# Optimization experiments

Hardware: AMD Instinct MI355X
Metric: run time of the kernel (lower is better)

The kernel has to match this reference:

```python
import jax, jax.numpy as jnp
import numpy as np

B, T, D, H, O = 8, 16, 113344, 512, 6


def setup_inputs() -> dict:
    key = jax.random.key(0)
    ks = jax.random.split(key, 11)
    k = 1.0 / np.sqrt(H)  # PyTorch nn.LSTM / nn.Linear default init scale
    u = lambda kk, shape: jax.random.uniform(kk, shape, jnp.float32, -k, k)
    x = jax.random.normal(ks[0], (B, T, D), jnp.float32)
    return dict(
        x=x,
        W_ih0=u(ks[1], (4 * H, D)), W_hh0=u(ks[2], (4 * H, H)),
        b_ih0=u(ks[3], (4 * H,)), b_hh0=u(ks[4], (4 * H,)),
        W_ih1=u(ks[5], (4 * H, H)), W_hh1=u(ks[6], (4 * H, H)),
        b_ih1=u(ks[7], (4 * H,)), b_hh1=u(ks[8], (4 * H,)),
        fc_w=u(ks[9], (O, H)), fc_b=u(ks[10], (O,)),
    )


def _lstm_layer(x, Wih, Whh, bih, bhh):
    # x: [B, T, D_in]; PyTorch gate order: i, f, g, o
    Bq = x.shape[0]
    Hq = Whh.shape[1]
    # Batch the input-to-hidden GEMM over all timesteps at once.
    xg = jnp.einsum('btd,gd->btg', x, Wih) + bih + bhh  # [B, T, 4H]

    def step(carry, xg_t):
        h, c = carry
        gates = xg_t + h @ Whh.T  # [B, 4H]
        i, f, g, o = jnp.split(gates, 4, axis=-1)
        i = jax.nn.sigmoid(i)
        f = jax.nn.sigmoid(f)
        g = jnp.tanh(g)
        o = jax.nn.sigmoid(o)
        c = f * c + i * g
        h = o * jnp.tanh(c)
        return (h, c), h

    h0 = jnp.zeros((Bq, Hq), x.dtype)
    c0 = jnp.zeros((Bq, Hq), x.dtype)
    (_, _), hs = jax.lax.scan(step, (h0, c0), jnp.swapaxes(xg, 0, 1))
    return jnp.swapaxes(hs, 0, 1)  # [B, T, H]


def reference(x, W_ih0, W_hh0, b_ih0, b_hh0, W_ih1, W_hh1, b_ih1, b_hh1, fc_w, fc_b):
    h = _lstm_layer(x, W_ih0, W_hh0, b_ih0, b_hh0)
    h = _lstm_layer(h, W_ih1, W_hh1, b_ih1, b_hh1)
    # fc on last timestep only
    return h[:, -1, :] @ fc_w.T + fc_b  # [B, O]
```

## Files before the change

kernel.cpp:

```cpp
#include <hip/hip_runtime.h>
#include <cstdint>
#include <cstddef>

typedef __attribute__((ext_vector_type(4))) float f32x4;
typedef __attribute__((ext_vector_type(8))) short s16x8;

#define MFMA16(a, b, c) __builtin_amdgcn_mfma_f32_16x16x32_bf16(a, b, c, 0, 0, 0)

__device__ __forceinline__ void bsplit(float f, unsigned short& h, unsigned short& l) {
  unsigned u = __float_as_uint(f);
  h = (unsigned short)(u >> 16);
  float hf = __uint_as_float(u & 0xffff0000u);
  l = (unsigned short)(__float_as_uint(f - hf) >> 16);
}

__device__ __forceinline__ void stage_tile(const float* __restrict__ base, int D, int k,
                                           unsigned short* ldsH, unsigned short* ldsL,
                                           int tid) {
#pragma unroll
  for (int v = 0; v < 4; ++v) {
    int flat = v * 256 + tid;
    int row = flat >> 3, kq = flat & 7;
    const float4 f = *(const float4*)(base + (size_t)row * D + k + kq * 4);
    ushort4 hh, ll;
    bsplit(f.x, hh.x, ll.x);
    bsplit(f.y, hh.y, ll.y);
    bsplit(f.z, hh.z, ll.z);
    bsplit(f.w, hh.w, ll.w);
    *(ushort4*)&ldsH[row * 40 + kq * 4] = hh;
    *(ushort4*)&ldsL[row * 40 + kq * 4] = ll;
  }
}

__global__ __launch_bounds__(256) void k_gemm(const float* __restrict__ A,
                                              const float* __restrict__ W,
                                              float* __restrict__ out,
                                              int D, int stepsPerChunk) {
  __shared__ __align__(16) unsigned short Ah[128 * 40], Al[128 * 40];
  __shared__ __align__(16) unsigned short Bh[128 * 40], Bl[128 * 40];
  const int tid = threadIdx.x;
  const int n0 = blockIdx.x * 128;
  const int totalSteps = D >> 5;
  const int s0 = blockIdx.y * stepsPerChunk;
  const int s1 = (s0 + stepsPerChunk < totalSteps) ? s0 + stepsPerChunk : totalSteps;
  const int wave = tid >> 6, lane = tid & 63;
  const int q = lane >> 4, li = lane & 15;
  const int wm = (wave >> 1) * 64, wn = (wave & 1) * 64;
  const float* bbase = W + (size_t)n0 * D;

  f32x4 acc[4][4] = {};

  for (int s = s0; s < s1; ++s) {
    const int k = s << 5;
    stage_tile(A, D, k, Ah, Al, tid);
    stage_tile(bbase, D, k, Bh, Bl, tid);
    __syncthreads();

    s16x8 a_h[4], a_l[4], b_h[4], b_l[4];
#pragma unroll
    for (int mt = 0; mt < 4; ++mt) {
      int m = wm + mt * 16 + li;
      a_h[mt] = *(const s16x8*)&Ah[m * 40 + q * 8];
      a_l[mt] = *(const s16x8*)&Al[m * 40 + q * 8];
    }
#pragma unroll
    for (int nt = 0; nt < 4; ++nt) {
      int n = wn + nt * 16 + li;
      b_h[nt] = *(const s16x8*)&Bh[n * 40 + q * 8];
      b_l[nt] = *(const s16x8*)&Bl[n * 40 + q * 8];
    }
#pragma unroll
    for (int mt = 0; mt < 4; ++mt)
#pragma unroll
      for (int nt = 0; nt < 4; ++nt) {
        acc[mt][nt] = MFMA16(a_h[mt], b_h[nt], acc[mt][nt]);
        acc[mt][nt] = MFMA16(a_h[mt], b_l[nt], acc[mt][nt]);
        acc[mt][nt] = MFMA16(a_l[mt], b_h[nt], acc[mt][nt]);
      }
    __syncthreads();
  }

#pragma unroll
  for (int mt = 0; mt < 4; ++mt)
#pragma unroll
    for (int nt = 0; nt < 4; ++nt)
#pragma unroll
      for (int r = 0; r < 4; ++r) {
        int m = wm + mt * 16 + q * 4 + r;
        int n = n0 + wn + nt * 16 + li;
        atomicAdd(&out[m * 2048 + n], acc[mt][nt][r]);
      }
}

__global__ __launch_bounds__(256) void k_rec(const float* __restrict__ xg,
                                             const float* __restrict__ Whh,
                                             const float* __restrict__ bih,
                                             const float* __restrict__ bhh,
                                             float* __restrict__ h_all,
                                             int* __restrict__ cnt) {
  __shared__ __align__(16) unsigned short Ah[16 * 520], Al[16 * 520];
  const int tid = threadIdx.x;
  const int lane = tid & 63, wave = tid >> 6;
  const int q = lane >> 4, li = lane & 15;
  const int g = li >> 2, jj = li & 3;
  const int wgl = blockIdx.x * 4 + wave;
  const int j0 = wgl * 4;
  const int row = g * 512 + j0 + jj;

  for (int i = tid; i < 16 * 520; i += 256) { Ah[i] = 0; Al[i] = 0; }

  s16x8 wh[16], wl[16];
#pragma unroll
  for (int ks = 0; ks < 16; ++ks) {
    float fv[8];
    *(float4*)&fv[0] = *(const float4*)(Whh + row * 512 + ks * 32 + q * 8);
    *(float4*)&fv[4] = *(const float4*)(Whh + row * 512 + ks * 32 + q * 8 + 4);
    s16x8 h8, l8;
#pragma unroll
    for (int j = 0; j < 8; ++j) {
      unsigned short h, l;
      bsplit(fv[j], h, l);
      h8[j] = (short)h;
      l8[j] = (short)l;
    }
    wh[ks] = h8;
    wl[ks] = l8;
  }
  const float bias = bih[row] + bhh[row];
  float c[4] = {0.f, 0.f, 0.f, 0.f};
  __syncthreads();

  for (int t = 0; t < 16; ++t) {
    if (t > 0) {
      if (tid == 0) {
        while (__hip_atomic_load(cnt + (t - 1), __ATOMIC_ACQUIRE,
                                 __HIP_MEMORY_SCOPE_AGENT) < (int)gridDim.x) {}
      }
      __syncthreads();
#pragma unroll
      for (int v = 0; v < 4; ++v) {
        int flat = v * 256 + tid;
        int b = flat >> 7, kq = flat & 127;
        float4 f = *(const float4*)(h_all + (b * 16 + (t - 1)) * 512 + kq * 4);
        ushort4 hh, ll;
        bsplit(f.x, hh.x, ll.x);
        bsplit(f.y, hh.y, ll.y);
        bsplit(f.z, hh.z, ll.z);
        bsplit(f.w, hh.w, ll.w);
        *(ushort4*)&Ah[b * 520 + kq * 4] = hh;
        *(ushort4*)&Al[b * 520 + kq * 4] = ll;
      }
      __syncthreads();
    }

    f32x4 acc = {0.f, 0.f, 0.f, 0.f};
    if (t > 0) {
#pragma unroll
      for (int ks = 0; ks < 16; ++ks) {
        s16x8 ah = *(const s16x8*)&Ah[li * 520 + ks * 32 + q * 8];
        s16x8 al = *(const s16x8*)&Al[li * 520 + ks * 32 + q * 8];
        acc = MFMA16(ah, wh[ks], acc);
        acc = MFMA16(ah, wl[ks], acc);
        acc = MFMA16(al, wh[ks], acc);
      }
    }

    float val[4];
#pragma unroll
    for (int r = 0; r < 4; ++r) {
      int mrow = q * 4 + r;
      float pre = acc[r] + bias;
      if (mrow < 8) pre += xg[(mrow * 16 + t) * 2048 + row];
      val[r] = (g == 2) ? tanhf(pre) : 1.f / (1.f + __expf(-pre));
    }
    const int base = lane & 48;
#pragma unroll
    for (int r = 0; r < 4; ++r) {
      float iv = __shfl(val[r], base + 0 + jj);
      float fv = __shfl(val[r], base + 4 + jj);
      float gv = __shfl(val[r], base + 8 + jj);
      float ov = __shfl(val[r], base + 12 + jj);
      int mrow = q * 4 + r;
      if (g == 0 && mrow < 8) {
        c[r] = fv * c[r] + iv * gv;
        float hv = ov * tanhf(c[r]);
        h_all[(mrow * 16 + t) * 512 + j0 + jj] = hv;
      }
    }

    if (t < 15) {
      __threadfence();
      __syncthreads();
      if (tid == 0)
        __hip_atomic_fetch_add(cnt + t, 1, __ATOMIC_RELEASE, __HIP_MEMORY_SCOPE_AGENT);
    }
  }
}

__global__ void k_fc(const float* __restrict__ h_all, const float* __restrict__ fw,
                     const float* __restrict__ fb, float* __restrict__ out) {
  int b = blockIdx.x / 6, o = blockIdx.x % 6;
  int lane = threadIdx.x;
  const float* h = h_all + (b * 16 + 15) * 512;
  float s = 0.f;
  for (int j = lane; j < 512; j += 64) s += h[j] * fw[o * 512 + j];
#pragma unroll
  for (int off = 32; off; off >>= 1) s += __shfl_down(s, off);
  if (lane == 0) out[b * 6 + o] = s + fb[o];
}

extern "C" void kernel_launch(void* const* d_in, const int* in_sizes, int n_in,
                              void* d_out, int out_size, void* d_ws, size_t ws_size,
                              hipStream_t stream) {
  const float* x    = (const float*)d_in[0];
  const float* Wih0 = (const float*)d_in[1];
  const float* Whh0 = (const float*)d_in[2];
  const float* bih0 = (const float*)d_in[3];
  const float* bhh0 = (const float*)d_in[4];
  const float* Wih1 = (const float*)d_in[5];
  const float* Whh1 = (const float*)d_in[6];
  const float* bih1 = (const float*)d_in[7];
  const float* bhh1 = (const float*)d_in[8];
  const float* fcw  = (const float*)d_in[9];
  const float* fcb  = (const float*)d_in[10];
  float* out = (float*)d_out;

  char* ws = (char*)d_ws;
  size_t off = 0;
  auto alloc = [&](size_t bytes) -> void* {
    void* p = ws + off;
    off += (bytes + 255) & ~(size_t)255;
    return p;
  };
  float* xg0 = (float*)alloc(128 * 2048 * sizeof(float));
  float* xg1 = (float*)alloc(128 * 2048 * sizeof(float));
  int* cnt   = (int*)alloc(4096);
  const size_t zeroBytes = off;
  float* h0 = (float*)alloc(128 * 512 * sizeof(float));
  float* h1 = (float*)alloc(128 * 512 * sizeof(float));
  (void)ws_size; (void)in_sizes; (void)n_in; (void)out_size;

  hipMemsetAsync(d_ws, 0, zeroBytes, stream);

  k_gemm<<<dim3(16, 77), 256, 0, stream>>>(x, Wih0, xg0, 113344, 46);
  k_rec<<<32, 256, 0, stream>>>(xg0, Whh0, bih0, bhh0, h0, cnt);

  k_gemm<<<dim3(16, 4), 256, 0, stream>>>(h0, Wih1, xg1, 512, 4);
  k_rec<<<32, 256, 0, stream>>>(xg1, Whh1, bih1, bhh1, h1, cnt + 16);

  k_fc<<<48, 64, 0, stream>>>(h1, fcw, fcb, out);
}
```

Baseline: 1.612 ms.

## Fuse both LSTM layers into one wavefront-pipelined kernel and prefetch GEMM tiles

```diff
diff --git a/kernel.cpp b/kernel.cpp
--- a/kernel.cpp
+++ b/kernel.cpp
@@ -14,14 +14,24 @@
   l = (unsigned short)(__float_as_uint(f - hf) >> 16);
 }
 
-__device__ __forceinline__ void stage_tile(const float* __restrict__ base, int D, int k,
-                                           unsigned short* ldsH, unsigned short* ldsL,
-                                           int tid) {
+
+__device__ __forceinline__ void load_tile(const float* __restrict__ base, int D, int k,
+                                          int tid, float4* r) {
 #pragma unroll
   for (int v = 0; v < 4; ++v) {
     int flat = v * 256 + tid;
     int row = flat >> 3, kq = flat & 7;
-    const float4 f = *(const float4*)(base + (size_t)row * D + k + kq * 4);
+    r[v] = *(const float4*)(base + (size_t)row * D + k + kq * 4);
+  }
+}
+
+__device__ __forceinline__ void write_tile(const float4* r, unsigned short* ldsH,
+                                           unsigned short* ldsL, int tid) {
+#pragma unroll
+  for (int v = 0; v < 4; ++v) {
+    int flat = v * 256 + tid;
+    int row = flat >> 3, kq = flat & 7;
+    float4 f = r[v];
     ushort4 hh, ll;
     bsplit(f.x, hh.x, ll.x);
     bsplit(f.y, hh.y, ll.y);
@@ -32,10 +42,10 @@
   }
 }
 
-__global__ __launch_bounds__(256) void k_gemm(const float* __restrict__ A,
-                                              const float* __restrict__ W,
-                                              float* __restrict__ out,
-                                              int D, int stepsPerChunk) {
+__global__ __launch_bounds__(256, 2) void k_gemm(const float* __restrict__ A,
+                                                 const float* __restrict__ W,
+                                                 float* __restrict__ out,
+                                                 int D, int stepsPerChunk) {
   __shared__ __align__(16) unsigned short Ah[128 * 40], Al[128 * 40];
   __shared__ __align__(16) unsigned short Bh[128 * 40], Bl[128 * 40];
   const int tid = threadIdx.x;
@@ -49,12 +59,18 @@
   const float* bbase = W + (size_t)n0 * D;
 
   f32x4 acc[4][4] = {};
+  float4 pa[4], pb[4];
+  load_tile(A, D, s0 << 5, tid, pa);
+  load_tile(bbase, D, s0 << 5, tid, pb);
 
   for (int s = s0; s < s1; ++s) {
-    const int k = s << 5;
-    stage_tile(A, D, k, Ah, Al, tid);
-    stage_tile(bbase, D, k, Bh, Bl, tid);
+    write_tile(pa, Ah, Al, tid);
+    write_tile(pb, Bh, Bl, tid);
     __syncthreads();
+    if (s + 1 < s1) {
+      load_tile(A, D, (s + 1) << 5, tid, pa);
+      load_tile(bbase, D, (s + 1) << 5, tid, pb);
+    }
 
     s16x8 a_h[4], a_l[4], b_h[4], b_l[4];
 #pragma unroll
@@ -92,29 +108,14 @@
       }
 }
 
-__global__ __launch_bounds__(256) void k_rec(const float* __restrict__ xg,
-                                             const float* __restrict__ Whh,
-                                             const float* __restrict__ bih,
-                                             const float* __restrict__ bhh,
-                                             float* __restrict__ h_all,
-                                             int* __restrict__ cnt) {
-  __shared__ __align__(16) unsigned short Ah[16 * 520], Al[16 * 520];
-  const int tid = threadIdx.x;
-  const int lane = tid & 63, wave = tid >> 6;
-  const int q = lane >> 4, li = lane & 15;
-  const int g = li >> 2, jj = li & 3;
-  const int wgl = blockIdx.x * 4 + wave;
-  const int j0 = wgl * 4;
-  const int row = g * 512 + j0 + jj;
-
-  for (int i = tid; i < 16 * 520; i += 256) { Ah[i] = 0; Al[i] = 0; }
-
-  s16x8 wh[16], wl[16];
+
+__device__ __forceinline__ void load_wfrags(const float* __restrict__ W, int row, int q,
+                                            s16x8* wh, s16x8* wl) {
 #pragma unroll
   for (int ks = 0; ks < 16; ++ks) {
     float fv[8];
-    *(float4*)&fv[0] = *(const float4*)(Whh + row * 512 + ks * 32 + q * 8);
-    *(float4*)&fv[4] = *(const float4*)(Whh + row * 512 + ks * 32 + q * 8 + 4);
+    *(float4*)&fv[0] = *(const float4*)(W + row * 512 + ks * 32 + q * 8);
+    *(float4*)&fv[4] = *(const float4*)(W + row * 512 + ks * 32 + q * 8 + 4);
     s16x8 h8, l8;
 #pragma unroll
     for (int j = 0; j < 8; ++j) {
@@ -126,73 +127,158 @@
     wh[ks] = h8;
     wl[ks] = l8;
   }
-  const float bias = bih[row] + bhh[row];
+}
+
+__device__ __forceinline__ void stage_h(const float* __restrict__ src, int t,
+                                        unsigned short* Ah, unsigned short* Al, int tid) {
+#pragma unroll
+  for (int v = 0; v < 4; ++v) {
+    int flat = v * 256 + tid;
+    int b = flat >> 7, kq = flat & 127;
+    float4 f = *(const float4*)(src + (b * 16 + t) * 512 + kq * 4);
+    ushort4 hh, ll;
+    bsplit(f.x, hh.x, ll.x);
+    bsplit(f.y, hh.y, ll.y);
+    bsplit(f.z, hh.z, ll.z);
+    bsplit(f.w, hh.w, ll.w);
+    *(ushort4*)&Ah[b * 520 + kq * 4] = hh;
+    *(ushort4*)&Al[b * 520 + kq * 4] = ll;
+  }
+}
+
+__device__ __forceinline__ f32x4 mac_tile(const unsigned short* Ah, const unsigned short* Al,
+                                          const s16x8* wh, const s16x8* wl,
+                                          int li, int q, f32x4 acc) {
+#pragma unroll
+  for (int ks = 0; ks < 16; ++ks) {
+    s16x8 ah = *(const s16x8*)&Ah[li * 520 + ks * 32 + q * 8];
+    s16x8 al = *(const s16x8*)&Al[li * 520 + ks * 32 + q * 8];
+    acc = MFMA16(ah, wh[ks], acc);
+    acc = MFMA16(ah, wl[ks], acc);
+    acc = MFMA16(al, wh[ks], acc);
+  }
+  return acc;
+}
+
+__global__ __launch_bounds__(256, 1) void k_rec2(
+    const float* __restrict__ xg0,
+    const float* __restrict__ Whh0,
+    const float* __restrict__ bih0, const float* __restrict__ bhh0,
+    const float* __restrict__ Wih1, const float* __restrict__ Whh1,
+    const float* __restrict__ bih1, const float* __restrict__ bhh1,
+    float* __restrict__ h0_all, float* __restrict__ h1_all,
+    int* __restrict__ cnt0, int* __restrict__ cnt1) {
+  __shared__ __align__(16) unsigned short A0h[16 * 520], A0l[16 * 520];
+  __shared__ __align__(16) unsigned short A1h[16 * 520], A1l[16 * 520];
+  const int tid = threadIdx.x;
+  const int lane = tid & 63, wave = tid >> 6;
+  const int q = lane >> 4, li = lane & 15;
+  const int g = li >> 2, jj = li & 3;
+  const int layer = blockIdx.x >> 5;
+  const int blk = blockIdx.x & 31;
+  const int wgl = blk * 4 + wave;
+  const int j0 = wgl * 4;
+  const int row = g * 512 + j0 + jj;
+
+  for (int i = tid; i < 16 * 520; i += 256) {
+    A0h[i] = 0; A0l[i] = 0; A1h[i] = 0; A1l[i] = 0;
+  }
+
+  s16x8 wh[16], wl[16];
+  load_wfrags(layer ? Whh1 : Whh0, row, q, wh, wl);
+  s16x8 uh[16], ul[16];
+  if (layer) load_wfrags(Wih1, row, q, uh, ul);
+  const float bias = layer ? (bih1[row] + bhh1[row]) : (bih0[row] + bhh0[row]);
   float c[4] = {0.f, 0.f, 0.f, 0.f};
   __syncthreads();
 
-  for (int t = 0; t < 16; ++t) {
-    if (t > 0) {
-      if (tid == 0) {
-        while (__hip_atomic_load(cnt + (t - 1), __ATOMIC_ACQUIRE,
-                                 __HIP_MEMORY_SCOPE_AGENT) < (int)gridDim.x) {}
-      }
-      __syncthreads();
-#pragma unroll
-      for (int v = 0; v < 4; ++v) {
-        int flat = v * 256 + tid;
-        int b = flat >> 7, kq = flat & 127;
-        float4 f = *(const float4*)(h_all + (b * 16 + (t - 1)) * 512 + kq * 4);
-        ushort4 hh, ll;
-        bsplit(f.x, hh.x, ll.x);
-        bsplit(f.y, hh.y, ll.y);
-        bsplit(f.z, hh.z, ll.z);
-        bsplit(f.w, hh.w, ll.w);
-        *(ushort4*)&Ah[b * 520 + kq * 4] = hh;
-        *(ushort4*)&Al[b * 520 + kq * 4] = ll;
-      }
-      __syncthreads();
-    }
-
-    f32x4 acc = {0.f, 0.f, 0.f, 0.f};
-    if (t > 0) {
-#pragma unroll
-      for (int ks = 0; ks < 16; ++ks) {
-        s16x8 ah = *(const s16x8*)&Ah[li * 520 + ks * 32 + q * 8];
-        s16x8 al = *(const s16x8*)&Al[li * 520 + ks * 32 + q * 8];
-        acc = MFMA16(ah, wh[ks], acc);
-        acc = MFMA16(ah, wl[ks], acc);
-        acc = MFMA16(al, wh[ks], acc);
-      }
-    }
-
-    float val[4];
-#pragma unroll
-    for (int r = 0; r < 4; ++r) {
-      int mrow = q * 4 + r;
-      float pre = acc[r] + bias;
-      if (mrow < 8) pre += xg[(mrow * 16 + t) * 2048 + row];
-      val[r] = (g == 2) ? tanhf(pre) : 1.f / (1.f + __expf(-pre));
-    }
-    const int base = lane & 48;
-#pragma unroll
-    for (int r = 0; r < 4; ++r) {
-      float iv = __shfl(val[r], base + 0 + jj);
-      float fv = __shfl(val[r], base + 4 + jj);
-      float gv = __shfl(val[r], base + 8 + jj);
-      float ov = __shfl(val[r], base + 12 + jj);
-      int mrow = q * 4 + r;
-      if (g == 0 && mrow < 8) {
-        c[r] = fv * c[r] + iv * gv;
-        float hv = ov * tanhf(c[r]);
-        h_all[(mrow * 16 + t) * 512 + j0 + jj] = hv;
-      }
-    }
-
-    if (t < 15) {
+  if (layer == 0) {
+    for (int t = 0; t < 16; ++t) {
+      if (t > 0) {
+        if (tid == 0) {
+          while (__hip_atomic_load(cnt0 + (t - 1), __ATOMIC_ACQUIRE,
+                                   __HIP_MEMORY_SCOPE_AGENT) < 32) {}
+        }
+        __syncthreads();
+        stage_h(h0_all, t - 1, A0h, A0l, tid);
+        __syncthreads();
+      }
+
+      f32x4 acc = {0.f, 0.f, 0.f, 0.f};
+      if (t > 0) acc = mac_tile(A0h, A0l, wh, wl, li, q, acc);
+
+      float val[4];
+#pragma unroll
+      for (int r = 0; r < 4; ++r) {
+        int mrow = q * 4 + r;
+        float pre = acc[r] + bias;
+        if (mrow < 8) pre += xg0[(mrow * 16 + t) * 2048 + row];
+        val[r] = (g == 2) ? tanhf(pre) : 1.f / (1.f + __expf(-pre));
+      }
+      const int base = lane & 48;
+#pragma unroll
+      for (int r = 0; r < 4; ++r) {
+        float iv = __shfl(val[r], base + 0 + jj);
+        float fv = __shfl(val[r], base + 4 + jj);
+        float gv = __shfl(val[r], base + 8 + jj);
+        float ov = __shfl(val[r], base + 12 + jj);
+        int mrow = q * 4 + r;
+        if (g == 0 && mrow < 8) {
+          c[r] = fv * c[r] + iv * gv;
+          h0_all[(mrow * 16 + t) * 512 + j0 + jj] = ov * tanhf(c[r]);
+        }
+      }
+
       __threadfence();
       __syncthreads();
       if (tid == 0)
-        __hip_atomic_fetch_add(cnt + t, 1, __ATOMIC_RELEASE, __HIP_MEMORY_SCOPE_AGENT);
+        __hip_atomic_fetch_add(cnt0 + t, 1, __ATOMIC_RELEASE, __HIP_MEMORY_SCOPE_AGENT);
+    }
+  } else {
+    for (int t = 0; t < 16; ++t) {
+      if (tid == 0) {
+        while (__hip_atomic_load(cnt0 + t, __ATOMIC_ACQUIRE,
+                                 __HIP_MEMORY_SCOPE_AGENT) < 32) {}
+        if (t > 0) {
+          while (__hip_atomic_load(cnt1 + (t - 1), __ATOMIC_ACQUIRE,
+                                   __HIP_MEMORY_SCOPE_AGENT) < 32) {}
+        }
+      }
+      __syncthreads();
+      stage_h(h0_all, t, A0h, A0l, tid);
+      if (t > 0) stage_h(h1_all, t - 1, A1h, A1l, tid);
+      __syncthreads();
+
+      f32x4 acc = {0.f, 0.f, 0.f, 0.f};
+      acc = mac_tile(A0h, A0l, uh, ul, li, q, acc);
+      if (t > 0) acc = mac_tile(A1h, A1l, wh, wl, li, q, acc);
+
+      float val[4];
+#pragma unroll
+      for (int r = 0; r < 4; ++r) {
+        float pre = acc[r] + bias;
+        val[r] = (g == 2) ? tanhf(pre) : 1.f / (1.f + __expf(-pre));
+      }
+      const int base = lane & 48;
+#pragma unroll
+      for (int r = 0; r < 4; ++r) {
+        float iv = __shfl(val[r], base + 0 + jj);
+        float fv = __shfl(val[r], base + 4 + jj);
+        float gv = __shfl(val[r], base + 8 + jj);
+        float ov = __shfl(val[r], base + 12 + jj);
+        int mrow = q * 4 + r;
+        if (g == 0 && mrow < 8) {
+          c[r] = fv * c[r] + iv * gv;
+          h1_all[(mrow * 16 + t) * 512 + j0 + jj] = ov * tanhf(c[r]);
+        }
+      }
+
+      if (t < 15) {
+        __threadfence();
+        __syncthreads();
+        if (tid == 0)
+          __hip_atomic_fetch_add(cnt1 + t, 1, __ATOMIC_RELEASE, __HIP_MEMORY_SCOPE_AGENT);
+      }
     }
   }
 }
@@ -233,7 +319,6 @@
     return p;
   };
   float* xg0 = (float*)alloc(128 * 2048 * sizeof(float));
-  float* xg1 = (float*)alloc(128 * 2048 * sizeof(float));
   int* cnt   = (int*)alloc(4096);
   const size_t zeroBytes = off;
   float* h0 = (float*)alloc(128 * 512 * sizeof(float));
@@ -243,10 +328,9 @@
   hipMemsetAsync(d_ws, 0, zeroBytes, stream);
 
   k_gemm<<<dim3(16, 77), 256, 0, stream>>>(x, Wih0, xg0, 113344, 46);
-  k_rec<<<32, 256, 0, stream>>>(xg0, Whh0, bih0, bhh0, h0, cnt);
-
-  k_gemm<<<dim3(16, 4), 256, 0, stream>>>(h0, Wih1, xg1, 512, 4);
-  k_rec<<<32, 256, 0, stream>>>(xg1, Whh1, bih1, bhh1, h1, cnt + 16);
+
+  k_rec2<<<64, 256, 0, stream>>>(xg0, Whh0, bih0, bhh0, Wih1, Whh1, bih1, bhh1,
+                                 h0, h1, cnt, cnt + 16);
 
   k_fc<<<48, 64, 0, stream>>>(h1, fcw, fcb, out);
 }
```

Measured after the change: 1.442 ms. 10.6% less time.
